# Kernel optimization log

Measured on AMD Instinct MI355X. Metric: run time of the kernel, lower is better.

## Reference

```python
import jax, jax.numpy as jnp
import numpy as np

N_NODES = 10000
N_EDGES = 640000
D_FEAT = 128
D_OUT = 128


def setup_inputs() -> dict:
    key = jax.random.key(0)
    k1, k2, k3, k4, k5 = jax.random.split(key, 5)
    h = jax.random.normal(k1, (N_NODES, D_FEAT), dtype=jnp.float32)
    norm = jax.random.uniform(k2, (N_NODES, 1), dtype=jnp.float32)
    # glorot-style scale for the dense weight (4*in_feats -> out_feats)
    weight = jax.random.normal(k3, (4 * D_FEAT, D_OUT), dtype=jnp.float32) * (2.0 / (4 * D_FEAT + D_OUT)) ** 0.5
    src = jax.random.randint(k4, (N_EDGES,), 0, N_NODES, dtype=jnp.int32)
    dst = jax.random.randint(k5, (N_EDGES,), 0, N_NODES, dtype=jnp.int32)
    return {"h": h, "norm": norm, "weight": weight, "src": src, "dst": dst}


def reference(h, norm, weight, src, dst):
    N = h.shape[0]
    # tf.math.l2_normalize: x * rsqrt(max(sum(x^2), 1e-12))
    h = h * jax.lax.rsqrt(jnp.maximum(jnp.sum(h * h, axis=-1, keepdims=True), 1e-12))
    h = h * norm  # [N, F]

    m = h[src]  # edge messages [E, F] (shared gather)

    # pass 1: copy_src + sum -> agg_h, then * norm
    agg_h = jax.ops.segment_sum(m, dst, num_segments=N) * norm

    # pass 2: mailbox max and mean(hard_sigmoid) over incoming messages
    deg = jax.ops.segment_sum(jnp.ones((m.shape[0],), dtype=h.dtype), dst, num_segments=N)  # [N]
    mx = jax.ops.segment_max(m, dst, num_segments=N)
    mx = jnp.where(deg[:, None] > 0, mx, 0.0)  # nodes w/o in-edges keep zeros
    # keras hard_sigmoid: clip(0.2*x + 0.5, 0, 1)
    hs_sum = jax.ops.segment_sum(jnp.clip(0.2 * m + 0.5, 0.0, 1.0), dst, num_segments=N)
    mean_hs = hs_sum / jnp.maximum(deg, 1.0)[:, None]
    accum_h = jnp.concatenate((mx, mean_hs), axis=1) * norm  # [N, 2F]

    out = jnp.concatenate((h, agg_h, accum_h), axis=1) @ weight  # [N, 4F] @ [4F, D_OUT]
    return jax.nn.relu(out)
```

## Files before the change

### kernel.cpp

```cpp
#include <hip/hip_runtime.h>
#include <math.h>

#define DF 128
#define DK 512
#define DO 128
#define CAP 128
#define CSTR 32

typedef __attribute__((ext_vector_type(8))) short bf16x8;
typedef __attribute__((ext_vector_type(8))) unsigned short u16x8;
typedef __attribute__((ext_vector_type(4))) float f32x4;
typedef __attribute__((ext_vector_type(2))) float f32x2;

__device__ inline unsigned short f2bf(float x) {
    unsigned int u = __builtin_bit_cast(unsigned int, x);
    unsigned int r = (u + 0x7FFFu + ((u >> 16) & 1u)) >> 16;
    return (unsigned short)r;
}

__global__ void prep_k(const float* __restrict__ W, unsigned short* __restrict__ Wt,
                       const float* __restrict__ h, const float* __restrict__ norm,
                       unsigned short* __restrict__ Xb, int* __restrict__ cur, int N) {
    int b = blockIdx.x;
    if (b < 32) {
        int t = b * 256 + threadIdx.x;
        int c  = t >> 6;
        int k0 = (t & 63) * 8;
        u16x8 v;
        #pragma unroll
        for (int j = 0; j < 8; ++j) v[j] = f2bf(W[(size_t)(k0 + j) * DO + c]);
        *reinterpret_cast<u16x8*>(Wt + (size_t)c * DK + k0) = v;
    } else {
        int wid = threadIdx.x >> 6;
        int t   = threadIdx.x & 63;
        int n   = (b - 32) * 4 + wid;
        if (n >= N) return;
        if (t == 0) cur[(size_t)n * CSTR] = 0;
        const float2 hv = reinterpret_cast<const float2*>(h + (size_t)n * DF)[t];
        float ss = hv.x * hv.x + hv.y * hv.y;
        #pragma unroll
        for (int o = 32; o > 0; o >>= 1) ss += __shfl_xor(ss, o);
        float scale = rsqrtf(fmaxf(ss, 1e-12f)) * norm[n];
        ushort2 o2;
        o2.x = f2bf(hv.x * scale);
        o2.y = f2bf(hv.y * scale);
        reinterpret_cast<ushort2*>(Xb + (size_t)n * DK)[t] = o2;
    }
}

__global__ void bucket_k(const int* __restrict__ src, const int* __restrict__ dst,
                         int* __restrict__ cur, unsigned short* __restrict__ bsrc, int E) {
    int t  = blockIdx.x * blockDim.x + threadIdx.x;
    int e0 = t * 4;
    if (e0 + 3 < E) {
        const int4 d4 = *reinterpret_cast<const int4*>(dst + e0);
        const int4 s4 = *reinterpret_cast<const int4*>(src + e0);
        int p0 = atomicAdd(&cur[(size_t)d4.x * CSTR], 1);
        int p1 = atomicAdd(&cur[(size_t)d4.y * CSTR], 1);
        int p2 = atomicAdd(&cur[(size_t)d4.z * CSTR], 1);
        int p3 = atomicAdd(&cur[(size_t)d4.w * CSTR], 1);
        if (p0 < CAP) bsrc[((size_t)d4.x << 7) + p0] = (unsigned short)s4.x;
        if (p1 < CAP) bsrc[((size_t)d4.y << 7) + p1] = (unsigned short)s4.y;
        if (p2 < CAP) bsrc[((size_t)d4.z << 7) + p2] = (unsigned short)s4.z;
        if (p3 < CAP) bsrc[((size_t)d4.w << 7) + p3] = (unsigned short)s4.w;
    } else {
        for (int e = e0; e < E; ++e) {
            int d = dst[e];
            int p = atomicAdd(&cur[(size_t)d * CSTR], 1);
            if (p < CAP) bsrc[((size_t)d << 7) + p] = (unsigned short)src[e];
        }
    }
}

__global__ void __launch_bounds__(512, 6) fused_k(const unsigned short* __restrict__ Xb,
                                                  const unsigned short* __restrict__ Wt,
                                                  const int* __restrict__ cur,
                                                  const float* __restrict__ norm,
                                                  const unsigned short* __restrict__ bsrc,
                                                  float* __restrict__ out, int N) {
    __shared__ unsigned short Xs[16][520];
    __shared__ unsigned short sid[8][128];
    int tid = threadIdx.x;
    int w = tid >> 6;
    int l = tid & 63;
    int nb0 = blockIdx.x * 8;
    int n = nb0 + w;
    int rq = l >> 4;
    int lc = l & 15;
    bool valid = (n < N);

    int cntt = valid ? cur[(size_t)n * CSTR] : 0;
    int cnt  = min(cntt, CAP);

    if (valid) {
        reinterpret_cast<unsigned int*>(&sid[w][0])[l] =
            reinterpret_cast<const unsigned int*>(bsrc + ((size_t)n << 7))[l];
        if (l < 16)
            *reinterpret_cast<u16x8*>(&Xs[w][lc * 8]) =
                *reinterpret_cast<const u16x8*>(Xb + (size_t)n * DK + lc * 8);
    }

    f32x2 s2[4], m2[4];
    #pragma unroll
    for (int q = 0; q < 4; ++q) {
        s2[q] = f32x2{0.0f, 0.0f};
        m2[q] = f32x2{-INFINITY, -INFINITY};
    }
    #pragma unroll 8
    for (int j = rq; j < cnt; j += 4) {
        int sj = (int)sid[w][j];
        uint4 v = *reinterpret_cast<const uint4*>(Xb + ((size_t)sj << 9) + lc * 8);
        #pragma unroll
        for (int q = 0; q < 4; ++q) {
            unsigned int wv = (&v.x)[q];
            f32x2 val;
            val.x = __builtin_bit_cast(float, wv << 16);
            val.y = __builtin_bit_cast(float, wv & 0xFFFF0000u);
            s2[q] += val;
            m2[q] = __builtin_elementwise_max(m2[q], val);
        }
    }

    float s[8], m[8];
    #pragma unroll
    for (int q = 0; q < 4; ++q) {
        s[2 * q] = s2[q].x;  s[2 * q + 1] = s2[q].y;
        m[2 * q] = m2[q].x;  m[2 * q + 1] = m2[q].y;
    }
    #pragma unroll
    for (int f = 0; f < 8; ++f) {
        s[f] += __shfl_xor(s[f], 16);
        s[f] += __shfl_xor(s[f], 32);
        m[f] = fmaxf(m[f], __shfl_xor(m[f], 16));
        m[f] = fmaxf(m[f], __shfl_xor(m[f], 32));
    }
    if (valid && l < 16) {
        float nm  = norm[n];
        float inv = 1.0f / fmaxf((float)cntt, 1.0f);
        u16x8 o1, o2, o3;
        #pragma unroll
        for (int f = 0; f < 8; ++f) {
            o1[f] = f2bf(s[f] * nm);
            float mm = (cnt > 0) ? m[f] : 0.0f;
            o2[f] = f2bf(mm * nm);
            o3[f] = f2bf((0.2f * s[f] + 0.5f * (float)cnt) * inv * nm);
        }
        *reinterpret_cast<u16x8*>(&Xs[w][128 + lc * 8]) = o1;
        *reinterpret_cast<u16x8*>(&Xs[w][256 + lc * 8]) = o2;
        *reinterpret_cast<u16x8*>(&Xs[w][384 + lc * 8]) = o3;
    }
    __syncthreads();

    int r  = l & 15;
    int kg = l >> 4;
    f32x4 acc = {};
    const unsigned short* B = Wt + (size_t)(w * 16 + r) * DK;
    #pragma unroll
    for (int ks = 0; ks < 16; ++ks) {
        bf16x8 a = *reinterpret_cast<const bf16x8*>(&Xs[r][ks * 32 + kg * 8]);
        bf16x8 b = *reinterpret_cast<const bf16x8*>(B + ks * 32 + kg * 8);
        acc = __builtin_amdgcn_mfma_f32_16x16x32_bf16(a, b, acc, 0, 0, 0);
    }
    if (kg < 2) {
        #pragma unroll
        for (int q = 0; q < 4; ++q) {
            int rr = nb0 + kg * 4 + q;
            if (rr < N) out[(size_t)rr * DO + w * 16 + r] = fmaxf(acc[q], 0.0f);
        }
    }
}

extern "C" void kernel_launch(void* const* d_in, const int* in_sizes, int n_in,
                              void* d_out, int out_size, void* d_ws, size_t ws_size,
                              hipStream_t stream) {
    const float* h    = (const float*)d_in[0];
    const float* norm = (const float*)d_in[1];
    const float* W    = (const float*)d_in[2];
    const int*   src  = (const int*)d_in[3];
    const int*   dst  = (const int*)d_in[4];
    float* out = (float*)d_out;

    int N = in_sizes[0] / DF;
    int E = in_sizes[3];

    unsigned short* Xb = (unsigned short*)d_ws;
    unsigned short* Wt = Xb + (size_t)N * DK;
    int* cur = (int*)(Wt + (size_t)DO * DK);
    unsigned short* bsrc = (unsigned short*)(cur + (size_t)N * CSTR);

    int nblk = (N + 3) / 4 + 32;
    prep_k  <<<dim3(nblk),              dim3(256), 0, stream>>>(W, Wt, h, norm, Xb, cur, N);
    bucket_k<<<dim3((E / 4 + 255)/256), dim3(256), 0, stream>>>(src, dst, cur, bsrc, E);
    fused_k <<<dim3((N + 7) / 8),       dim3(512), 0, stream>>>(Xb, Wt, cur, norm, bsrc, out, N);
}
```

Before: 74.90 us.

## Process 16 nodes per block and pad gather loop with duplicate neighbor ids

```diff
diff --git a/kernel.cpp b/kernel.cpp
--- a/kernel.cpp
+++ b/kernel.cpp
@@ -72,82 +72,105 @@
     }
 }
 
-__global__ void __launch_bounds__(512, 6) fused_k(const unsigned short* __restrict__ Xb,
-                                                  const unsigned short* __restrict__ Wt,
-                                                  const int* __restrict__ cur,
-                                                  const float* __restrict__ norm,
-                                                  const unsigned short* __restrict__ bsrc,
-                                                  float* __restrict__ out, int N) {
+__global__ void __launch_bounds__(512) fused_k(const unsigned short* __restrict__ Xb,
+                                               const unsigned short* __restrict__ Wt,
+                                               const int* __restrict__ cur,
+                                               const float* __restrict__ norm,
+                                               const unsigned short* __restrict__ bsrc,
+                                               float* __restrict__ out, int N) {
     __shared__ unsigned short Xs[16][520];
-    __shared__ unsigned short sid[8][128];
+    __shared__ unsigned short sid[16][128];
     int tid = threadIdx.x;
     int w = tid >> 6;
     int l = tid & 63;
-    int nb0 = blockIdx.x * 8;
-    int n = nb0 + w;
+    int nb0 = blockIdx.x * 16;
     int rq = l >> 4;
     int lc = l & 15;
-    bool valid = (n < N);
-
-    int cntt = valid ? cur[(size_t)n * CSTR] : 0;
-    int cnt  = min(cntt, CAP);
-
-    if (valid) {
-        reinterpret_cast<unsigned int*>(&sid[w][0])[l] =
+
+    for (int i = 0; i < 2; ++i) {
+        int ni = w * 2 + i;
+        int n  = nb0 + ni;
+        if (n >= N) continue;
+        int cntt = cur[(size_t)n * CSTR];
+        int cnt  = min(cntt, CAP);
+        reinterpret_cast<unsigned int*>(&sid[ni][0])[l] =
             reinterpret_cast<const unsigned int*>(bsrc + ((size_t)n << 7))[l];
         if (l < 16)
-            *reinterpret_cast<u16x8*>(&Xs[w][lc * 8]) =
+            *reinterpret_cast<u16x8*>(&Xs[ni][lc * 8]) =
                 *reinterpret_cast<const u16x8*>(Xb + (size_t)n * DK + lc * 8);
-    }
-
-    f32x2 s2[4], m2[4];
-    #pragma unroll
-    for (int q = 0; q < 4; ++q) {
-        s2[q] = f32x2{0.0f, 0.0f};
-        m2[q] = f32x2{-INFINITY, -INFINITY};
-    }
-    #pragma unroll 8
-    for (int j = rq; j < cnt; j += 4) {
-        int sj = (int)sid[w][j];
-        uint4 v = *reinterpret_cast<const uint4*>(Xb + ((size_t)sj << 9) + lc * 8);
+
+        int lastid = 0;
+        if (cnt > 0) {
+            lastid = (int)sid[ni][cnt - 1];
+            if (l >= cnt) sid[ni][l] = (unsigned short)lastid;
+            if (l + 64 >= cnt) sid[ni][l + 64] = (unsigned short)lastid;
+        }
+
+        f32x2 s2[4], m2[4];
         #pragma unroll
         for (int q = 0; q < 4; ++q) {
-            unsigned int wv = (&v.x)[q];
-            f32x2 val;
-            val.x = __builtin_bit_cast(float, wv << 16);
-            val.y = __builtin_bit_cast(float, wv & 0xFFFF0000u);
-            s2[q] += val;
-            m2[q] = __builtin_elementwise_max(m2[q], val);
-        }
-    }
-
-    float s[8], m[8];
-    #pragma unroll
-    for (int q = 0; q < 4; ++q) {
-        s[2 * q] = s2[q].x;  s[2 * q + 1] = s2[q].y;
-        m[2 * q] = m2[q].x;  m[2 * q + 1] = m2[q].y;
-    }
-    #pragma unroll
-    for (int f = 0; f < 8; ++f) {
-        s[f] += __shfl_xor(s[f], 16);
-        s[f] += __shfl_xor(s[f], 32);
-        m[f] = fmaxf(m[f], __shfl_xor(m[f], 16));
-        m[f] = fmaxf(m[f], __shfl_xor(m[f], 32));
-    }
-    if (valid && l < 16) {
-        float nm  = norm[n];
-        float inv = 1.0f / fmaxf((float)cntt, 1.0f);
-        u16x8 o1, o2, o3;
+            s2[q] = f32x2{0.0f, 0.0f};
+            m2[q] = f32x2{-INFINITY, -INFINITY};
+        }
+        int T = (cnt > 0) ? ((((cnt + 3) >> 2) + 7) & ~7) : 0;
+        #pragma unroll 8
+        for (int jj = 0; jj < T; ++jj) {
+            int j  = rq + 4 * jj;
+            int sj = (int)sid[ni][j];
+            uint4 v = *reinterpret_cast<const uint4*>(Xb + ((size_t)sj << 9) + lc * 8);
+            #pragma unroll
+            for (int q = 0; q < 4; ++q) {
+                unsigned int wv = (&v.x)[q];
+                f32x2 val;
+                val.x = __builtin_bit_cast(float, wv << 16);
+                val.y = __builtin_bit_cast(float, wv & 0xFFFF0000u);
+                s2[q] += val;
+                m2[q] = __builtin_elementwise_max(m2[q], val);
+            }
+        }
+        if (cnt > 0) {
+            int true_q = (cnt > rq) ? ((cnt - rq + 3) >> 2) : 0;
+            int kq = T - true_q;
+            if (kq > 0) {
+                uint4 v = *reinterpret_cast<const uint4*>(Xb + ((size_t)lastid << 9) + lc * 8);
+                float kf = (float)kq;
+                #pragma unroll
+                for (int q = 0; q < 4; ++q) {
+                    unsigned int wv = (&v.x)[q];
+                    s2[q].x -= kf * __builtin_bit_cast(float, wv << 16);
+                    s2[q].y -= kf * __builtin_bit_cast(float, wv & 0xFFFF0000u);
+                }
+            }
+        }
+
+        float s[8], m[8];
+        #pragma unroll
+        for (int q = 0; q < 4; ++q) {
+            s[2 * q] = s2[q].x;  s[2 * q + 1] = s2[q].y;
+            m[2 * q] = m2[q].x;  m[2 * q + 1] = m2[q].y;
+        }
         #pragma unroll
         for (int f = 0; f < 8; ++f) {
-            o1[f] = f2bf(s[f] * nm);
-            float mm = (cnt > 0) ? m[f] : 0.0f;
-            o2[f] = f2bf(mm * nm);
-            o3[f] = f2bf((0.2f * s[f] + 0.5f * (float)cnt) * inv * nm);
-        }
-        *reinterpret_cast<u16x8*>(&Xs[w][128 + lc * 8]) = o1;
-        *reinterpret_cast<u16x8*>(&Xs[w][256 + lc * 8]) = o2;
-        *reinterpret_cast<u16x8*>(&Xs[w][384 + lc * 8]) = o3;
+            s[f] += __shfl_xor(s[f], 16);
+            s[f] += __shfl_xor(s[f], 32);
+            m[f] = fmaxf(m[f], __shfl_xor(m[f], 16));
+            m[f] = fmaxf(m[f], __shfl_xor(m[f], 32));
+        }
+        if (l < 16) {
+            float nm  = norm[n];
+            float inv = 1.0f / fmaxf((float)cntt, 1.0f);
+            u16x8 o1, o2, o3;
+            #pragma unroll
+            for (int f = 0; f < 8; ++f) {
+                o1[f] = f2bf(s[f] * nm);
+                float mm = (cnt > 0) ? m[f] : 0.0f;
+                o2[f] = f2bf(mm * nm);
+                o3[f] = f2bf((0.2f * s[f] + 0.5f * (float)cnt) * inv * nm);
+            }
+            *reinterpret_cast<u16x8*>(&Xs[ni][128 + lc * 8]) = o1;
+            *reinterpret_cast<u16x8*>(&Xs[ni][256 + lc * 8]) = o2;
+            *reinterpret_cast<u16x8*>(&Xs[ni][384 + lc * 8]) = o3;
+        }
     }
     __syncthreads();
 
@@ -161,12 +184,10 @@
         bf16x8 b = *reinterpret_cast<const bf16x8*>(B + ks * 32 + kg * 8);
         acc = __builtin_amdgcn_mfma_f32_16x16x32_bf16(a, b, acc, 0, 0, 0);
     }
-    if (kg < 2) {
-        #pragma unroll
-        for (int q = 0; q < 4; ++q) {
-            int rr = nb0 + kg * 4 + q;
-            if (rr < N) out[(size_t)rr * DO + w * 16 + r] = fmaxf(acc[q], 0.0f);
-        }
+    #pragma unroll
+    for (int q = 0; q < 4; ++q) {
+        int rr = nb0 + kg * 4 + q;
+        if (rr < N) out[(size_t)rr * DO + w * 16 + r] = fmaxf(acc[q], 0.0f);
     }
 }
 
@@ -191,5 +212,5 @@
     int nblk = (N + 3) / 4 + 32;
     prep_k  <<<dim3(nblk),              dim3(256), 0, stream>>>(W, Wt, h, norm, Xb, cur, N);
     bucket_k<<<dim3((E / 4 + 255)/256), dim3(256), 0, stream>>>(src, dst, cur, bsrc, E);
-    fused_k <<<dim3((N + 7) / 8),       dim3(512), 0, stream>>>(Xb, Wt, cur, norm, bsrc, out, N);
-}
+    fused_k <<<dim3((N + 15) / 16),     dim3(512), 0, stream>>>(Xb, Wt, cur, norm, bsrc, out, N);
+}
```

After: 78.92 us. 1.05x slower.

## Split per-node mailboxes into source-range slices and process 16 nodes per block

Applied to the files above, without the earlier changes.

```diff
diff --git a/kernel.cpp b/kernel.cpp
--- a/kernel.cpp
+++ b/kernel.cpp
@@ -4,7 +4,9 @@
 #define DF 128
 #define DK 512
 #define DO 128
-#define CAP 128
+#define NS 4
+#define CAPS 40
+#define MST (NS * CAPS)
 #define CSTR 32
 
 typedef __attribute__((ext_vector_type(8))) short bf16x8;
@@ -35,7 +37,7 @@
         int t   = threadIdx.x & 63;
         int n   = (b - 32) * 4 + wid;
         if (n >= N) return;
-        if (t == 0) cur[(size_t)n * CSTR] = 0;
+        if (t < NS) cur[((size_t)n * NS + t) * CSTR] = 0;
         const float2 hv = reinterpret_cast<const float2*>(h + (size_t)n * DF)[t];
         float ss = hv.x * hv.x + hv.y * hv.y;
         #pragma unroll
@@ -49,52 +51,67 @@
 }
 
 __global__ void bucket_k(const int* __restrict__ src, const int* __restrict__ dst,
-                         int* __restrict__ cur, unsigned short* __restrict__ bsrc, int E) {
+                         int* __restrict__ cur, unsigned short* __restrict__ bsrc,
+                         int E, float sinv) {
     int t  = blockIdx.x * blockDim.x + threadIdx.x;
     int e0 = t * 4;
     if (e0 + 3 < E) {
         const int4 d4 = *reinterpret_cast<const int4*>(dst + e0);
         const int4 s4 = *reinterpret_cast<const int4*>(src + e0);
-        int p0 = atomicAdd(&cur[(size_t)d4.x * CSTR], 1);
-        int p1 = atomicAdd(&cur[(size_t)d4.y * CSTR], 1);
-        int p2 = atomicAdd(&cur[(size_t)d4.z * CSTR], 1);
-        int p3 = atomicAdd(&cur[(size_t)d4.w * CSTR], 1);
-        if (p0 < CAP) bsrc[((size_t)d4.x << 7) + p0] = (unsigned short)s4.x;
-        if (p1 < CAP) bsrc[((size_t)d4.y << 7) + p1] = (unsigned short)s4.y;
-        if (p2 < CAP) bsrc[((size_t)d4.z << 7) + p2] = (unsigned short)s4.z;
-        if (p3 < CAP) bsrc[((size_t)d4.w << 7) + p3] = (unsigned short)s4.w;
+        int sl0 = min(NS - 1, (int)((float)s4.x * sinv));
+        int sl1 = min(NS - 1, (int)((float)s4.y * sinv));
+        int sl2 = min(NS - 1, (int)((float)s4.z * sinv));
+        int sl3 = min(NS - 1, (int)((float)s4.w * sinv));
+        int p0 = atomicAdd(&cur[((size_t)d4.x * NS + sl0) * CSTR], 1);
+        int p1 = atomicAdd(&cur[((size_t)d4.y * NS + sl1) * CSTR], 1);
+        int p2 = atomicAdd(&cur[((size_t)d4.z * NS + sl2) * CSTR], 1);
+        int p3 = atomicAdd(&cur[((size_t)d4.w * NS + sl3) * CSTR], 1);
+        if (p0 < CAPS) bsrc[(size_t)d4.x * MST + sl0 * CAPS + p0] = (unsigned short)s4.x;
+        if (p1 < CAPS) bsrc[(size_t)d4.y * MST + sl1 * CAPS + p1] = (unsigned short)s4.y;
+        if (p2 < CAPS) bsrc[(size_t)d4.z * MST + sl2 * CAPS + p2] = (unsigned short)s4.z;
+        if (p3 < CAPS) bsrc[(size_t)d4.w * MST + sl3 * CAPS + p3] = (unsigned short)s4.w;
     } else {
         for (int e = e0; e < E; ++e) {
-            int d = dst[e];
-            int p = atomicAdd(&cur[(size_t)d * CSTR], 1);
-            if (p < CAP) bsrc[((size_t)d << 7) + p] = (unsigned short)src[e];
-        }
-    }
-}
-
-__global__ void __launch_bounds__(512, 6) fused_k(const unsigned short* __restrict__ Xb,
-                                                  const unsigned short* __restrict__ Wt,
-                                                  const int* __restrict__ cur,
-                                                  const float* __restrict__ norm,
-                                                  const unsigned short* __restrict__ bsrc,
-                                                  float* __restrict__ out, int N) {
+            int d  = dst[e];
+            int sv = src[e];
+            int sl = min(NS - 1, (int)((float)sv * sinv));
+            int p = atomicAdd(&cur[((size_t)d * NS + sl) * CSTR], 1);
+            if (p < CAPS) bsrc[(size_t)d * MST + sl * CAPS + p] = (unsigned short)sv;
+        }
+    }
+}
+
+__global__ void __launch_bounds__(1024) fused_k(const unsigned short* __restrict__ Xb,
+                                                const unsigned short* __restrict__ Wt,
+                                                const int* __restrict__ cur,
+                                                const float* __restrict__ norm,
+                                                const unsigned short* __restrict__ bsrc,
+                                                float* __restrict__ out, int N) {
     __shared__ unsigned short Xs[16][520];
-    __shared__ unsigned short sid[8][128];
+    __shared__ unsigned short sid[16][MST];
     int tid = threadIdx.x;
     int w = tid >> 6;
     int l = tid & 63;
-    int nb0 = blockIdx.x * 8;
+    int nb0 = blockIdx.x * 16;
     int n = nb0 + w;
     int rq = l >> 4;
     int lc = l & 15;
     bool valid = (n < N);
 
-    int cntt = valid ? cur[(size_t)n * CSTR] : 0;
-    int cnt  = min(cntt, CAP);
+    int craw[NS], cclamp[NS];
+    int cntt = 0;
+    #pragma unroll
+    for (int s = 0; s < NS; ++s) {
+        craw[s] = valid ? cur[((size_t)n * NS + s) * CSTR] : 0;
+        cclamp[s] = min(craw[s], CAPS);
+        cntt += craw[s];
+    }
 
     if (valid) {
-        reinterpret_cast<unsigned int*>(&sid[w][0])[l] =
-            reinterpret_cast<const unsigned int*>(bsrc + ((size_t)n << 7))[l];
+        const unsigned int* mb = reinterpret_cast<const unsigned int*>(bsrc + (size_t)n * MST);
+        unsigned int* sd = reinterpret_cast<unsigned int*>(&sid[w][0]);
+        sd[l] = mb[l];
+        if (l < MST / 2 - 64) sd[l + 64] = mb[l + 64];
         if (l < 16)
             *reinterpret_cast<u16x8*>(&Xs[w][lc * 8]) =
                 *reinterpret_cast<const u16x8*>(Xb + (size_t)n * DK + lc * 8);
@@ -106,18 +123,22 @@
         s2[q] = f32x2{0.0f, 0.0f};
         m2[q] = f32x2{-INFINITY, -INFINITY};
     }
-    #pragma unroll 8
-    for (int j = rq; j < cnt; j += 4) {
-        int sj = (int)sid[w][j];
-        uint4 v = *reinterpret_cast<const uint4*>(Xb + ((size_t)sj << 9) + lc * 8);
-        #pragma unroll
-        for (int q = 0; q < 4; ++q) {
-            unsigned int wv = (&v.x)[q];
-            f32x2 val;
-            val.x = __builtin_bit_cast(float, wv << 16);
-            val.y = __builtin_bit_cast(float, wv & 0xFFFF0000u);
-            s2[q] += val;
-            m2[q] = __builtin_elementwise_max(m2[q], val);
+    for (int s = 0; s < NS; ++s) {
+        int base = s * CAPS;
+        int cs   = cclamp[s];
+        #pragma unroll 4
+        for (int j = rq; j < cs; j += 4) {
+            int sj = (int)sid[w][base + j];
+            uint4 v = *reinterpret_cast<const uint4*>(Xb + ((size_t)sj << 9) + lc * 8);
+            #pragma unroll
+            for (int q = 0; q < 4; ++q) {
+                unsigned int wv = (&v.x)[q];
+                f32x2 val;
+                val.x = __builtin_bit_cast(float, wv << 16);
+                val.y = __builtin_bit_cast(float, wv & 0xFFFF0000u);
+                s2[q] += val;
+                m2[q] = __builtin_elementwise_max(m2[q], val);
+            }
         }
     }
 
@@ -141,9 +162,9 @@
         #pragma unroll
         for (int f = 0; f < 8; ++f) {
             o1[f] = f2bf(s[f] * nm);
-            float mm = (cnt > 0) ? m[f] : 0.0f;
+            float mm = (cntt > 0) ? m[f] : 0.0f;
             o2[f] = f2bf(mm * nm);
-            o3[f] = f2bf((0.2f * s[f] + 0.5f * (float)cnt) * inv * nm);
+            o3[f] = f2bf((0.2f * s[f] + 0.5f * (float)cntt) * inv * nm);
         }
         *reinterpret_cast<u16x8*>(&Xs[w][128 + lc * 8]) = o1;
         *reinterpret_cast<u16x8*>(&Xs[w][256 + lc * 8]) = o2;
@@ -151,17 +172,17 @@
     }
     __syncthreads();
 
-    int r  = l & 15;
-    int kg = l >> 4;
-    f32x4 acc = {};
-    const unsigned short* B = Wt + (size_t)(w * 16 + r) * DK;
-    #pragma unroll
-    for (int ks = 0; ks < 16; ++ks) {
-        bf16x8 a = *reinterpret_cast<const bf16x8*>(&Xs[r][ks * 32 + kg * 8]);
-        bf16x8 b = *reinterpret_cast<const bf16x8*>(B + ks * 32 + kg * 8);
-        acc = __builtin_amdgcn_mfma_f32_16x16x32_bf16(a, b, acc, 0, 0, 0);
-    }
-    if (kg < 2) {
+    if (w < 8) {
+        int r  = l & 15;
+        int kg = l >> 4;
+        f32x4 acc = {};
+        const unsigned short* B = Wt + (size_t)(w * 16 + r) * DK;
+        #pragma unroll
+        for (int ks = 0; ks < 16; ++ks) {
+            bf16x8 a = *reinterpret_cast<const bf16x8*>(&Xs[r][ks * 32 + kg * 8]);
+            bf16x8 b = *reinterpret_cast<const bf16x8*>(B + ks * 32 + kg * 8);
+            acc = __builtin_amdgcn_mfma_f32_16x16x32_bf16(a, b, acc, 0, 0, 0);
+        }
         #pragma unroll
         for (int q = 0; q < 4; ++q) {
             int rr = nb0 + kg * 4 + q;
@@ -186,10 +207,12 @@
     unsigned short* Xb = (unsigned short*)d_ws;
     unsigned short* Wt = Xb + (size_t)N * DK;
     int* cur = (int*)(Wt + (size_t)DO * DK);
-    unsigned short* bsrc = (unsigned short*)(cur + (size_t)N * CSTR);
+    unsigned short* bsrc = (unsigned short*)(cur + (size_t)N * NS * CSTR);
+
+    float sinv = (float)NS / (float)N;
 
     int nblk = (N + 3) / 4 + 32;
-    prep_k  <<<dim3(nblk),              dim3(256), 0, stream>>>(W, Wt, h, norm, Xb, cur, N);
-    bucket_k<<<dim3((E / 4 + 255)/256), dim3(256), 0, stream>>>(src, dst, cur, bsrc, E);
-    fused_k <<<dim3((N + 7) / 8),       dim3(512), 0, stream>>>(Xb, Wt, cur, norm, bsrc, out, N);
-}
+    prep_k  <<<dim3(nblk),              dim3(256),  0, stream>>>(W, Wt, h, norm, Xb, cur, N);
+    bucket_k<<<dim3((E / 4 + 255)/256), dim3(256),  0, stream>>>(src, dst, cur, bsrc, E, sinv);
+    fused_k <<<dim3((N + 15) / 16),     dim3(1024), 0, stream>>>(Xb, Wt, cur, norm, bsrc, out, N);
+}
```

Result: no change. 75.19 us (+0.4%).
